# Kernel optimization log

Hardware: AMD Instinct MI355X
Metric: run time of the kernel (lower is better)

The kernel has to match this reference:

```python
import jax, jax.numpy as jnp
import numpy as np

# pywt 'haar': dec_lo = [1/sqrt2, 1/sqrt2], dec_hi = [-1/sqrt2, 1/sqrt2]
_SQ = np.float32(1.0 / np.sqrt(2.0))
_DEC_LO = np.array([_SQ, _SQ], dtype=np.float32)
_DEC_HI = np.array([-_SQ, _SQ], dtype=np.float32)


def _make_filter():
    ll = np.outer(_DEC_LO, _DEC_LO)
    lh = np.outer(_DEC_HI, _DEC_LO)
    hl = np.outer(_DEC_LO, _DEC_HI)
    hh = np.outer(_DEC_HI, _DEC_HI)
    # torch code writes filters flipped ([::-1, ::-1]) then uses cross-correlation
    f = np.stack([ll, lh, hl, hh], axis=0)[:, ::-1, ::-1]  # [4, 2, 2]
    return jnp.asarray(np.ascontiguousarray(f))


def setup_inputs() -> dict:
    key = jax.random.key(0)
    x = jax.random.normal(key, (8, 64, 256, 256), dtype=jnp.float32)
    return {"x": x}


def reference(x):
    B, C, H, W = x.shape
    filt = _make_filter()  # [4, 2, 2]
    # The torch module's split/pad/conv3d/split/cat pipeline is equivalent to a
    # depthwise 2x2 conv producing 4 subbands per channel, ordered
    # [c0:(LL,LH,HL,HH), c1:(LL,LH,HL,HH), ...] along the channel dim.
    kernel = jnp.tile(filt[None], (C, 1, 1, 1)).reshape(C * 4, 1, 2, 2)
    # F.pad(..., (0,1,0,1)): pad right and bottom by 1 with zeros
    xp = jnp.pad(x, ((0, 0), (0, 0), (0, 1), (0, 1)))
    out = jax.lax.conv_general_dilated(
        xp, kernel,
        window_strides=(1, 1),
        padding='VALID',
        dimension_numbers=('NCHW', 'OIHW', 'NCHW'),
        feature_group_count=C,
    )
    return out  # [B, 4*C, H, W]
```

## Files before the change

kernel.cpp:

```cpp
#include <hip/hip_runtime.h>


constexpr int Bn = 8, Cn = 64, Hn = 256, Wn = 256;
constexpr int ROWS_PER_BLOCK = 4;

__global__ __launch_bounds__(256)
void haar_dwt_kernel(const float* __restrict__ x, float* __restrict__ out) {
    const int tid  = threadIdx.x;
    const int lane = tid & 63;
    const int rib  = tid >> 6;

    const int rows_groups = Hn / ROWS_PER_BLOCK;
    const int rg  = blockIdx.x % rows_groups;
    const int bc  = blockIdx.x / rows_groups;
    const int row = rg * ROWS_PER_BLOCK + rib;
    const int j0  = lane * 4;

    const size_t plane_elems = (size_t)Hn * Wn;
    const float* plane = x + (size_t)bc * plane_elems;

    const float* p0 = plane + (size_t)row * Wn + j0;
    float4 r0 = *reinterpret_cast<const float4*>(p0);
    float  e0 = (j0 + 4 < Wn) ? p0[4] : 0.0f;

    float4 r1 = make_float4(0.f, 0.f, 0.f, 0.f);
    float  e1 = 0.0f;
    if (row + 1 < Hn) {
        const float* p1 = p0 + Wn;
        r1 = *reinterpret_cast<const float4*>(p1);
        e1 = (j0 + 4 < Wn) ? p1[4] : 0.0f;
    }

    float a0[5] = {r0.x, r0.y, r0.z, r0.w, e0};
    float a1[5] = {r1.x, r1.y, r1.z, r1.w, e1};

    float4 vll, vlh, vhl, vhh;
    float* pll = reinterpret_cast<float*>(&vll);
    float* plh = reinterpret_cast<float*>(&vlh);
    float* phl = reinterpret_cast<float*>(&vhl);
    float* phh = reinterpret_cast<float*>(&vhh);

#pragma unroll
    for (int k = 0; k < 4; ++k) {
        const float x00 = a0[k], x01 = a0[k + 1];
        const float x10 = a1[k], x11 = a1[k + 1];
        const float sum0 = x00 + x01;
        const float dif0 = x00 - x01;
        const float sum1 = x10 + x11;
        const float dif1 = x10 - x11;
        pll[k] = 0.5f * (sum0 + sum1);
        plh[k] = 0.5f * (sum0 - sum1);
        phl[k] = 0.5f * (dif0 + dif1);
        phh[k] = 0.5f * (dif0 - dif1);
    }

    const int b = bc / Cn;
    const int c = bc % Cn;
    float* obase = out + ((size_t)(b * 4 * Cn + 4 * c)) * plane_elems
                       + (size_t)row * Wn + j0;

    *reinterpret_cast<float4*>(obase)                   = vll;
    *reinterpret_cast<float4*>(obase + plane_elems)     = vlh;
    *reinterpret_cast<float4*>(obase + 2 * plane_elems) = vhl;
    *reinterpret_cast<float4*>(obase + 3 * plane_elems) = vhh;
}

extern "C" void kernel_launch(void* const* d_in, const int* in_sizes, int n_in,
                              void* d_out, int out_size, void* d_ws, size_t ws_size,
                              hipStream_t stream) {
    const float* x = (const float*)d_in[0];
    float* out = (float*)d_out;

    const int grid = Bn * Cn * (Hn / ROWS_PER_BLOCK);
    haar_dwt_kernel<<<grid, 256, 0, stream>>>(x, out);
}
```

Before: 598.1 us.

## Process four rows per wave with shuffle-based halo and nontemporal stores

Each wave now computes four consecutive output rows from five loaded input rows, so every input row is reused across adjacent outputs instead of being loaded twice. The right-neighbour element comes from a lane shuffle rather than a separate scalar global load. Outputs are written with nontemporal stores so the large write stream does not pollute cache. The grid shrinks fourfold and each thread holds more registers, which lowers block count and occupancy.

```diff
diff --git a/kernel.cpp b/kernel.cpp
--- a/kernel.cpp
+++ b/kernel.cpp
@@ -1,68 +1,71 @@
 #include <hip/hip_runtime.h>
 
 
+typedef float f4 __attribute__((ext_vector_type(4)));
+
 constexpr int Bn = 8, Cn = 64, Hn = 256, Wn = 256;
-constexpr int ROWS_PER_BLOCK = 4;
+constexpr int ROWS_PER_WAVE  = 4;
+constexpr int WAVES_PER_BLOCK = 4;
+constexpr int ROWS_PER_BLOCK = ROWS_PER_WAVE * WAVES_PER_BLOCK;
 
 __global__ __launch_bounds__(256)
 void haar_dwt_kernel(const float* __restrict__ x, float* __restrict__ out) {
     const int tid  = threadIdx.x;
     const int lane = tid & 63;
-    const int rib  = tid >> 6;
+    const int wave = tid >> 6;
 
-    const int rows_groups = Hn / ROWS_PER_BLOCK;
-    const int rg  = blockIdx.x % rows_groups;
-    const int bc  = blockIdx.x / rows_groups;
-    const int row = rg * ROWS_PER_BLOCK + rib;
-    const int j0  = lane * 4;
+    const int groups = Hn / ROWS_PER_BLOCK;
+    const int g  = blockIdx.x % groups;
+    const int bc = blockIdx.x / groups;
+    const int row0 = g * ROWS_PER_BLOCK + wave * ROWS_PER_WAVE;
+    const int j0   = lane * 4;
 
-    const size_t plane_elems = (size_t)Hn * Wn;
-    const float* plane = x + (size_t)bc * plane_elems;
+    const size_t plane = (size_t)Hn * Wn;
+    const float* pbase = x + (size_t)bc * plane + (size_t)row0 * Wn + j0;
 
-    const float* p0 = plane + (size_t)row * Wn + j0;
-    float4 r0 = *reinterpret_cast<const float4*>(p0);
-    float  e0 = (j0 + 4 < Wn) ? p0[4] : 0.0f;
-
-    float4 r1 = make_float4(0.f, 0.f, 0.f, 0.f);
-    float  e1 = 0.0f;
-    if (row + 1 < Hn) {
-        const float* p1 = p0 + Wn;
-        r1 = *reinterpret_cast<const float4*>(p1);
-        e1 = (j0 + 4 < Wn) ? p1[4] : 0.0f;
-    }
-
-    float a0[5] = {r0.x, r0.y, r0.z, r0.w, e0};
-    float a1[5] = {r1.x, r1.y, r1.z, r1.w, e1};
-
-    float4 vll, vlh, vhl, vhh;
-    float* pll = reinterpret_cast<float*>(&vll);
-    float* plh = reinterpret_cast<float*>(&vlh);
-    float* phl = reinterpret_cast<float*>(&vhl);
-    float* phh = reinterpret_cast<float*>(&vhh);
-
+    f4 in[5];
+    float e[5];
 #pragma unroll
-    for (int k = 0; k < 4; ++k) {
-        const float x00 = a0[k], x01 = a0[k + 1];
-        const float x10 = a1[k], x11 = a1[k + 1];
-        const float sum0 = x00 + x01;
-        const float dif0 = x00 - x01;
-        const float sum1 = x10 + x11;
-        const float dif1 = x10 - x11;
-        pll[k] = 0.5f * (sum0 + sum1);
-        plh[k] = 0.5f * (sum0 - sum1);
-        phl[k] = 0.5f * (dif0 + dif1);
-        phh[k] = 0.5f * (dif0 - dif1);
+    for (int t = 0; t < 5; ++t) {
+        const int r = row0 + t;
+        if (r < Hn) {
+            in[t] = *reinterpret_cast<const f4*>(pbase + (size_t)t * Wn);
+        } else {
+            in[t] = (f4){0.f, 0.f, 0.f, 0.f};
+        }
+        const float nb = __shfl_down(in[t][0], 1, 64);
+        e[t] = (lane == 63) ? 0.0f : nb;
     }
 
     const int b = bc / Cn;
     const int c = bc % Cn;
-    float* obase = out + ((size_t)(b * 4 * Cn + 4 * c)) * plane_elems
-                       + (size_t)row * Wn + j0;
+    float* ob = out + ((size_t)(b * 4 * Cn + 4 * c)) * plane
+                    + (size_t)row0 * Wn + j0;
 
-    *reinterpret_cast<float4*>(obase)                   = vll;
-    *reinterpret_cast<float4*>(obase + plane_elems)     = vlh;
-    *reinterpret_cast<float4*>(obase + 2 * plane_elems) = vhl;
-    *reinterpret_cast<float4*>(obase + 3 * plane_elems) = vhh;
+#pragma unroll
+    for (int t = 0; t < ROWS_PER_WAVE; ++t) {
+        f4 vll, vlh, vhl, vhh;
+#pragma unroll
+        for (int k = 0; k < 4; ++k) {
+            const float x00 = in[t][k];
+            const float x01 = (k < 3) ? in[t][k + 1] : e[t];
+            const float x10 = in[t + 1][k];
+            const float x11 = (k < 3) ? in[t + 1][k + 1] : e[t + 1];
+            const float sum0 = x00 + x01;
+            const float dif0 = x00 - x01;
+            const float sum1 = x10 + x11;
+            const float dif1 = x10 - x11;
+            vll[k] = 0.5f * (sum0 + sum1);
+            vlh[k] = 0.5f * (sum0 - sum1);
+            vhl[k] = 0.5f * (dif0 + dif1);
+            vhh[k] = 0.5f * (dif0 - dif1);
+        }
+        float* o = ob + (size_t)t * Wn;
+        __builtin_nontemporal_store(vll, reinterpret_cast<f4*>(o));
+        __builtin_nontemporal_store(vlh, reinterpret_cast<f4*>(o + plane));
+        __builtin_nontemporal_store(vhl, reinterpret_cast<f4*>(o + 2 * plane));
+        __builtin_nontemporal_store(vhh, reinterpret_cast<f4*>(o + 3 * plane));
+    }
 }
 
 extern "C" void kernel_launch(void* const* d_in, const int* in_sizes, int n_in,
```

Result: slower. 616.8 us (+3.1%).
